# Optimization experiments

Hardware: AMD Instinct MI355X
Metric: run time of the kernel (lower is better)

Reference implementation:

```python
import jax, jax.numpy as jnp
import numpy as np

N = 100000   # nodes
E = 300000   # edges per snapshot
S = 5        # snapshots
D_IN = 128   # node_dim
H = 256      # hidden dim
P = 10000    # post nodes


def setup_inputs() -> dict:
    key = jax.random.key(0)
    ks = jax.random.split(key, 8)
    node_features = jax.random.normal(ks[0], (N, D_IN), jnp.float32)
    edge_index = jax.random.randint(ks[1], (S, 2, E), 0, N, dtype=jnp.int64)
    post_idx = jax.random.randint(ks[2], (P,), 0, N, dtype=jnp.int64)
    glorot = lambda k, sh, fan: jax.random.normal(k, sh, jnp.float32) * (1.0 / np.sqrt(fan))
    return {
        'node_features': node_features,
        'edge_index': edge_index,
        'post_idx': post_idx,
        'W1': glorot(ks[3], (D_IN, H), D_IN), 'b1': jnp.zeros((H,), jnp.float32),
        'W2': glorot(ks[4], (H, H), H),       'b2': jnp.zeros((H,), jnp.float32),
        'Wc1': glorot(ks[5], (H, H // 2), H), 'bc1': jnp.zeros((H // 2,), jnp.float32),
        'Wc2': glorot(ks[6], (H // 2, 1), H // 2), 'bc2': jnp.zeros((1,), jnp.float32),
    }


def gcn_conv(x, src, dst, W, b):
    """PyG GCNConv: h = D^-1/2 (A+I) D^-1/2 (x W) + b, aggregate at target (dst)."""
    n = x.shape[0]
    h = x @ W                                   # [n, out]
    loop = jnp.arange(n, dtype=src.dtype)
    src2 = jnp.concatenate([src, loop])          # add self-loops
    dst2 = jnp.concatenate([dst, loop])
    deg = jax.ops.segment_sum(jnp.ones_like(dst2, jnp.float32), dst2, num_segments=n)
    dinv = jnp.where(deg > 0, jax.lax.rsqrt(deg), 0.0)
    norm = dinv[src2] * dinv[dst2]               # [E+n]
    out = jax.ops.segment_sum(h[src2] * norm[:, None], dst2, num_segments=n)
    return out + b


def reference(node_features, edge_index, post_idx, W1, b1, W2, b2, Wc1, bc1, Wc2, bc2):
    embs = []
    for s in range(edge_index.shape[0]):  # loop over fixed small snapshot count
        src, dst = edge_index[s, 0], edge_index[s, 1]
        # layer 0: 128 -> 256, relu, no skip (dims differ)
        x1 = jax.nn.relu(gcn_conv(node_features, src, dst, W1, b1))
        # layer 1 (last): 256 -> 256, no relu, residual skip
        x2 = gcn_conv(x1, src, dst, W2, b2) + x1
        embs.append(x2)
    agg = jnp.mean(jnp.stack(embs, axis=0), axis=0)  # mean over snapshots
    post = agg[post_idx]                             # [P, H]
    logits = jax.nn.relu(post @ Wc1 + bc1) @ Wc2 + bc2
    return jax.nn.sigmoid(logits[:, 0])              # [P]
```

## Files before the change

### kernel.cpp

```cpp
#include <hip/hip_runtime.h>
#include <hip/hip_bf16.h>
#include <math.h>

#define NN 100000
#define NE 300000
#define NS 5
#define DIN 128
#define HID 256
#define NP 10000
#define NB_N 391

#define NBUCK 1024
#define NBUCK_USED 782
#define PBLK 64
#define EPB 19
#define BCAP 2048
#define CAPR 40960
#define NCPAD 16
#define LDB 136

typedef short s8v __attribute__((ext_vector_type(8)));
typedef float f4v __attribute__((ext_vector_type(4)));

static __device__ __forceinline__ float bf2f(unsigned short u) {
    union { unsigned int i; float f; } v; v.i = ((unsigned int)u) << 16; return v.f;
}
static __device__ __forceinline__ unsigned short f2bf(float f) {
    union { float f; unsigned int i; } v; v.f = f;
    return (unsigned short)((v.i + 0x7fff + ((v.i >> 16) & 1)) >> 16);
}


__global__ void setpost_kernel(const int* __restrict__ post, int* __restrict__ isPost,
                               int* __restrict__ needed) {
    int i = blockIdx.x * 256 + threadIdx.x;
    int s = blockIdx.y;
    if (i < NP) {
        int nd = post[i];
        needed[(size_t)s * NN + nd] = 1;
        if (s == 0) isPost[nd] = 1;
    }
}


__global__ void prep_kernel(const float* __restrict__ X, unsigned short* __restrict__ Xb,
                            const float* __restrict__ W1, unsigned short* __restrict__ W1t,
                            const float* __restrict__ W2, unsigned short* __restrict__ W2t,
                            const float* __restrict__ Wc1, unsigned short* __restrict__ Wc1t) {
    int b = blockIdx.x, t = threadIdx.x;
    if (b < 12500) {
        int i = b * 256 + t;
        float4 v = *(const float4*)&X[(size_t)i * 4];
        ushort4 o;
        o.x = f2bf(v.x); o.y = f2bf(v.y); o.z = f2bf(v.z); o.w = f2bf(v.w);
        *(ushort4*)&Xb[(size_t)i * 4] = o;
    } else if (b < 12628) {
        int i = (b - 12500) * 256 + t;
        int n = i >> 7, k = i & 127;
        W1t[i] = f2bf(W1[(size_t)k * 256 + n]);
    } else if (b < 12884) {
        int i = (b - 12628) * 256 + t;
        int n = i >> 8, k = i & 255;
        W2t[i] = f2bf(W2[(size_t)k * 256 + n]);
    } else {
        int i = (b - 12884) * 256 + t;
        int n = i >> 8, k = i & 255;
        Wc1t[i] = f2bf(Wc1[(size_t)k * 128 + n]);
    }
}


__global__ void hist_kernel(const int* __restrict__ EI, int* __restrict__ bhist) {
    __shared__ int h[NBUCK];
    int s = blockIdx.y, b = blockIdx.x, t = threadIdx.x;
    for (int q = t; q < NBUCK; q += 256) h[q] = 0;
    __syncthreads();
    const int* dstp = EI + (size_t)s * 2 * NE + NE;
    int e0 = b * (EPB * 256);
    #pragma unroll
    for (int j = 0; j < EPB; j++) {
        int e = e0 + j * 256 + t;
        if (e < NE) atomicAdd(&h[dstp[e] >> 7], 1);
    }
    __syncthreads();
    for (int q = t; q < NBUCK; q += 256)
        if (h[q]) atomicAdd(&bhist[s * NBUCK + q], h[q]);
}

__global__ void bscan_kernel(const int* __restrict__ bhist, int* __restrict__ bbase,
                             int* __restrict__ bcur) {
    __shared__ int sm[NBUCK];
    int s = blockIdx.x, t = threadIdx.x;
    int v = bhist[s * NBUCK + t];
    sm[t] = v;
    __syncthreads();
    for (int d = 1; d < NBUCK; d <<= 1) {
        int x = (t >= d) ? sm[t - d] : 0;
        __syncthreads();
        sm[t] += x;
        __syncthreads();
    }
    int base = sm[t] - v;
    bbase[s * NBUCK + t] = base;
    bcur[s * NBUCK + t] = base;
}

__global__ void part_kernel(const int* __restrict__ EI, int* __restrict__ bcur,
                            int2* __restrict__ pairs) {
    __shared__ int h[NBUCK];
    __shared__ int base[NBUCK];
    int s = blockIdx.y, b = blockIdx.x, t = threadIdx.x;
    for (int q = t; q < NBUCK; q += 256) h[q] = 0;
    __syncthreads();
    const int* srcp = EI + (size_t)s * 2 * NE;
    const int* dstp = srcp + NE;
    int e0 = b * (EPB * 256);
    int rs[EPB], rd[EPB];
    #pragma unroll
    for (int j = 0; j < EPB; j++) {
        int e = e0 + j * 256 + t;
        if (e < NE) {
            rs[j] = srcp[e];
            rd[j] = dstp[e];
            atomicAdd(&h[rd[j] >> 7], 1);
        } else {
            rd[j] = -1; rs[j] = 0;
        }
    }
    __syncthreads();
    for (int q = t; q < NBUCK; q += 256) {
        int c = h[q];
        base[q] = c ? atomicAdd(&bcur[s * NBUCK + q], c) : 0;
    }
    __syncthreads();
    #pragma unroll
    for (int j = 0; j < EPB; j++) {
        if (rd[j] >= 0) {
            int pos = atomicAdd(&base[rd[j] >> 7], 1);
            pairs[(size_t)s * NE + pos] = make_int2(rs[j], rd[j]);
        }
    }
}

__global__ void bucket_csr_kernel(const int2* __restrict__ pairs, const int* __restrict__ bbase,
                                  const int* __restrict__ bhist, const int* __restrict__ isPost,
                                  int* __restrict__ cnt, int* __restrict__ offs,
                                  float* __restrict__ dinv, int* __restrict__ csr,
                                  int* __restrict__ needed) {
    __shared__ int nh[128];
    __shared__ int noff[128];
    __shared__ int sbuf[BCAP];
    int s = blockIdx.y, b = blockIdx.x, t = threadIdx.x;
    int base = bbase[s * NBUCK + b];
    int count = bhist[s * NBUCK + b];
    if (count > BCAP) count = BCAP;
    if (t < 128) nh[t] = 0;
    __syncthreads();
    const int2* pp = pairs + (size_t)s * NE + base;
    for (int e = t; e < count; e += 256)
        atomicAdd(&nh[pp[e].y & 127], 1);
    __syncthreads();
    if (t < 128) noff[t] = nh[t];
    __syncthreads();
    for (int d = 1; d < 128; d <<= 1) {
        int x = 0;
        if (t < 128 && t >= d) x = noff[t - d];
        __syncthreads();
        if (t < 128) noff[t] += x;
        __syncthreads();
    }
    if (t < 128) {
        int excl = noff[t] - nh[t];
        noff[t] = excl;
        int g = b * 128 + t;
        if (g < NN) {
            int c = nh[t];
            cnt[(size_t)s * NN + g]  = c;
            offs[(size_t)s * NN + g] = base + excl;
            dinv[(size_t)s * NN + g] = rsqrtf((float)(c + 1));
        }
    }
    __syncthreads();
    for (int e = t; e < count; e += 256) {
        int2 pr = pp[e];
        int pos = atomicAdd(&noff[pr.y & 127], 1);
        sbuf[pos] = pr.x;
        if (isPost[pr.y]) needed[(size_t)s * NN + pr.x] = 1;
    }
    __syncthreads();
    for (int e = t; e < count; e += 256)
        csr[(size_t)s * NE + base + e] = sbuf[e];
}


__global__ void compact_kernel(const int* __restrict__ needed, int* __restrict__ ncount,
                               int* __restrict__ list, int* __restrict__ inv) {
    __shared__ int wcnt[4];
    __shared__ int gbase;
    int s = blockIdx.y;
    int i = blockIdx.x * 256 + threadIdx.x;
    int wave = threadIdx.x >> 6, lane = threadIdx.x & 63;
    bool pred = (i < NN) && (needed[(size_t)s * NN + i] != 0);
    unsigned long long mask = __ballot(pred);
    int wc = __popcll(mask);
    if (lane == 0) wcnt[wave] = wc;
    __syncthreads();
    if (threadIdx.x == 0) {
        int tot = wcnt[0] + wcnt[1] + wcnt[2] + wcnt[3];
        gbase = tot ? atomicAdd(&ncount[s * NCPAD], tot) : 0;
    }
    __syncthreads();
    if (pred) {
        int wbase = gbase;
        #pragma unroll
        for (int q = 0; q < 4; q++) if (q < wave) wbase += wcnt[q];
        int rank = __popcll(mask & ((1ull << lane) - 1ull));
        int slot = wbase + rank;
        if (slot < CAPR) {
            list[(size_t)s * NN + slot] = i;
            inv[(size_t)s * NN + i] = slot;
        }
    }
}


__global__ __launch_bounds__(1024) void agg_mm1_kernel(
        const unsigned short* __restrict__ Xb, const unsigned short* __restrict__ W1t,
        const int* __restrict__ ncount, const float* __restrict__ dinvA,
        const int* __restrict__ offsA, const int* __restrict__ cntA,
        const int* __restrict__ csrA, const int* __restrict__ listA,
        const float* __restrict__ b1, unsigned short* __restrict__ x1cA) {
    int s = blockIdx.y;
    int M = ncount[s * NCPAD];
    if (M > CAPR) M = CAPR;
    if (blockIdx.x * 256 >= M) return;
    const float* dinv = dinvA + (size_t)s * NN;
    const int* offs = offsA + (size_t)s * NN;
    const int* cnt  = cntA + (size_t)s * NN;
    const int* csr  = csrA + (size_t)s * NE;
    const int* list = listA + (size_t)s * NN;
    unsigned short* x1c = x1cA + (size_t)s * CAPR * HID;

    __shared__ unsigned short ldsB[256 * LDB];
    int tid = threadIdx.x;
    for (int q = tid; q < 256 * 16; q += 1024) {
        int n = q >> 4;
        int k8 = (q & 15) * 8;
        *(s8v*)&ldsB[n * LDB + k8] = *(const s8v*)&W1t[n * 128 + k8];
    }
    __syncthreads();

    int wave = tid >> 6, lane = tid & 63, lr = lane & 15, g = lane >> 4;
    int rowbase = blockIdx.x * 256 + wave * 16;
    int arow = rowbase + lr;

    float ga[4][8];
    #pragma unroll
    for (int kk = 0; kk < 4; kk++)
        #pragma unroll
        for (int j = 0; j < 8; j++) ga[kk][j] = 0.f;
    float di = 0.f;

    if (arow < M) {
        int node = list[arow];
        int o = offs[node], c = cnt[node];
        di = dinv[node];
        const unsigned short* rp = Xb + (size_t)node * DIN + g * 8;
        #pragma unroll
        for (int kk = 0; kk < 4; kk++) {
            s8v h = *(const s8v*)(rp + kk * 32);
            #pragma unroll
            for (int j = 0; j < 8; j++) ga[kk][j] = di * bf2f((unsigned short)h[j]);
        }
        for (int k = 0; k < c; k++) {
            int sv = csr[o + k];
            float wgt = dinv[sv];
            const unsigned short* sp = Xb + (size_t)sv * DIN + g * 8;
            #pragma unroll
            for (int kk = 0; kk < 4; kk++) {
                s8v h = *(const s8v*)(sp + kk * 32);
                #pragma unroll
                for (int j = 0; j < 8; j++) ga[kk][j] += wgt * bf2f((unsigned short)h[j]);
            }
        }
    }

    f4v acc[16];
    #pragma unroll
    for (int t8 = 0; t8 < 16; t8++) acc[t8] = (f4v){0.f, 0.f, 0.f, 0.f};
    #pragma unroll
    for (int kk = 0; kk < 4; kk++) {
        s8v a;
        #pragma unroll
        for (int j = 0; j < 8; j++) a[j] = (short)f2bf(ga[kk][j]);
        #pragma unroll
        for (int t8 = 0; t8 < 16; t8++) {
            s8v b = *(const s8v*)&ldsB[(t8 * 16 + lr) * LDB + kk * 32 + g * 8];
            acc[t8] = __builtin_amdgcn_mfma_f32_16x16x32_bf16(a, b, acc[t8], 0, 0, 0);
        }
    }

    int orow0 = rowbase + g * 4;
    #pragma unroll
    for (int r = 0; r < 4; r++) {
        int row = orow0 + r;
        float sc = __shfl(di, g * 4 + r, 64);
        if (row < M) {
            #pragma unroll
            for (int t8 = 0; t8 < 16; t8++) {
                int col = t8 * 16 + lr;
                float v = sc * acc[t8][r] + b1[col];
                x1c[(size_t)row * HID + col] = f2bf(v > 0.f ? v : 0.f);
            }
        }
    }
}


__global__ void z2_kernel(const unsigned short* __restrict__ x1cA, const float* __restrict__ dinvA,
                          const int* __restrict__ offsA, const int* __restrict__ cntA,
                          const int* __restrict__ csrA, const int* __restrict__ invA,
                          const int* __restrict__ post, unsigned short* __restrict__ z2bA) {
    int s = blockIdx.y;
    const unsigned short* x1c = x1cA + (size_t)s * CAPR * HID;
    const float* dinv = dinvA + (size_t)s * NN;
    const int* offs = offsA + (size_t)s * NN;
    const int* cnt  = cntA + (size_t)s * NN;
    const int* csr  = csrA + (size_t)s * NE;
    const int* inv  = invA + (size_t)s * NN;
    unsigned short* z2b = z2bA + (size_t)s * NP * HID;

    int wave = threadIdx.x >> 6, lane = threadIdx.x & 63;
    int eg = lane >> 4, el = lane & 15;
    int p = blockIdx.x * 4 + wave;
    if (p >= NP) return;
    int node = post[p];
    int o = offs[node], c = cnt[node];
    float acc0[8] = {0.f, 0.f, 0.f, 0.f, 0.f, 0.f, 0.f, 0.f};
    float acc1[8] = {0.f, 0.f, 0.f, 0.f, 0.f, 0.f, 0.f, 0.f};
    for (int k = eg; k < c; k += 4) {
        int sv = csr[o + k];
        float wgt = dinv[sv];
        int r = inv[sv];
        const unsigned short* rp = &x1c[(size_t)r * HID + el * 16];
        s8v h0 = *(const s8v*)rp;
        s8v h1 = *(const s8v*)(rp + 8);
        #pragma unroll
        for (int j = 0; j < 8; j++) {
            acc0[j] += wgt * bf2f((unsigned short)h0[j]);
            acc1[j] += wgt * bf2f((unsigned short)h1[j]);
        }
    }
    if (eg == 0) {
        float di = dinv[node];
        int r = inv[node];
        const unsigned short* rp = &x1c[(size_t)r * HID + el * 16];
        s8v h0 = *(const s8v*)rp;
        s8v h1 = *(const s8v*)(rp + 8);
        #pragma unroll
        for (int j = 0; j < 8; j++) {
            acc0[j] += di * bf2f((unsigned short)h0[j]);
            acc1[j] += di * bf2f((unsigned short)h1[j]);
        }
    }
    #pragma unroll
    for (int j = 0; j < 8; j++) {
        acc0[j] += __shfl_xor(acc0[j], 16, 64);
        acc0[j] += __shfl_xor(acc0[j], 32, 64);
        acc1[j] += __shfl_xor(acc1[j], 16, 64);
        acc1[j] += __shfl_xor(acc1[j], 32, 64);
    }
    if (eg == 0) {
        s8v o0, o1;
        #pragma unroll
        for (int j = 0; j < 8; j++) {
            o0[j] = (short)f2bf(acc0[j]);
            o1[j] = (short)f2bf(acc1[j]);
        }
        unsigned short* wp = &z2b[(size_t)p * HID + el * 16];
        *(s8v*)wp = o0;
        *(s8v*)(wp + 8) = o1;
    }
}


__global__ __launch_bounds__(1024) void mm2_kernel(
        const unsigned short* __restrict__ z2bA,
        const unsigned short* __restrict__ W2t,
        const float* __restrict__ dinvA,
        const int* __restrict__ post,
        const int* __restrict__ invA,
        const float* __restrict__ b2,
        const unsigned short* __restrict__ x1cA,
        float* __restrict__ aggPA) {
    int s = blockIdx.z;
    const unsigned short* A = z2bA + (size_t)s * NP * HID;
    const float* dinv = dinvA + (size_t)s * NN;
    const int* inv = invA + (size_t)s * NN;
    const unsigned short* x1c = x1cA + (size_t)s * CAPR * HID;
    float* Out = aggPA + (size_t)s * NP * HID;

    __shared__ unsigned short lds[128 * (HID + 8)];
    int tid = threadIdx.x;
    int colbase = blockIdx.y * 128;
    for (int q = tid; q < 128 * 32; q += 1024) {
        int n = q >> 5;
        int k8 = (q & 31) * 8;
        *(s8v*)&lds[n * (HID + 8) + k8] = *(const s8v*)&W2t[(size_t)(colbase + n) * HID + k8];
    }
    __syncthreads();

    int wave = tid >> 6, lane = tid & 63, lr = lane & 15, g = lane >> 4;
    int rowbase = blockIdx.x * 256 + wave * 16;
    int arow = rowbase + lr;

    f4v acc[8];
    #pragma unroll
    for (int t = 0; t < 8; t++) acc[t] = (f4v){0.f, 0.f, 0.f, 0.f};

    #pragma unroll
    for (int kk = 0; kk < HID / 32; kk++) {
        s8v a = (s8v){0, 0, 0, 0, 0, 0, 0, 0};
        if (arow < NP) a = *(const s8v*)&A[(size_t)arow * HID + kk * 32 + g * 8];
        #pragma unroll
        for (int t = 0; t < 8; t++) {
            s8v b = *(const s8v*)&lds[(t * 16 + lr) * (HID + 8) + kk * 32 + g * 8];
            acc[t] = __builtin_amdgcn_mfma_f32_16x16x32_bf16(a, b, acc[t], 0, 0, 0);
        }
    }

    int orow0 = rowbase + g * 4;
    #pragma unroll
    for (int r = 0; r < 4; r++) {
        int row = orow0 + r;
        if (row < NP) {
            int nd = post[row];
            float sc = dinv[nd];
            size_t x1row = (size_t)inv[nd] * HID;
            #pragma unroll
            for (int t = 0; t < 8; t++) {
                int col = colbase + t * 16 + lr;
                Out[(size_t)row * HID + col] =
                    sc * acc[t][r] + b2[col] + bf2f(x1c[x1row + col]);
            }
        }
    }
}


__global__ void redcvt_kernel(const float* __restrict__ aggPA, unsigned short* __restrict__ aggPb) {
    int i = blockIdx.x * 256 + threadIdx.x;
    if (i < NP * HID / 4) {
        float4 a = *(const float4*)&aggPA[(size_t)i * 4];
        #pragma unroll
        for (int s = 1; s < NS; s++) {
            float4 b = *(const float4*)&aggPA[(size_t)s * NP * HID + (size_t)i * 4];
            a.x += b.x; a.y += b.y; a.z += b.z; a.w += b.w;
        }
        ushort4 o;
        o.x = f2bf(a.x); o.y = f2bf(a.y); o.z = f2bf(a.z); o.w = f2bf(a.w);
        *(ushort4*)&aggPb[(size_t)i * 4] = o;
    }
}


__global__ __launch_bounds__(256) void mm3f_kernel(
        const unsigned short* __restrict__ A, const unsigned short* __restrict__ Bt,
        const float* __restrict__ bc1, const float* __restrict__ Wc2,
        const float* __restrict__ bc2, float* __restrict__ out) {
    __shared__ float tile[64 * 133];
    __shared__ float wc2s[128];
    int tid = threadIdx.x;
    if (tid < 128) wc2s[tid] = Wc2[tid];
    int wave = tid >> 6, lane = tid & 63, lr = lane & 15, g = lane >> 4;
    int rowbase = blockIdx.x * 64 + wave * 16;
    int arow = rowbase + lr;

    f4v acc[8];
    #pragma unroll
    for (int t = 0; t < 8; t++) acc[t] = (f4v){0.f, 0.f, 0.f, 0.f};

    #pragma unroll
    for (int kk = 0; kk < HID / 32; kk++) {
        s8v a = (s8v){0, 0, 0, 0, 0, 0, 0, 0};
        if (arow < NP) a = *(const s8v*)&A[(size_t)arow * HID + kk * 32 + g * 8];
        #pragma unroll
        for (int t = 0; t < 8; t++) {
            s8v b = *(const s8v*)&Bt[(size_t)(t * 16 + lr) * HID + kk * 32 + g * 8];
            acc[t] = __builtin_amdgcn_mfma_f32_16x16x32_bf16(a, b, acc[t], 0, 0, 0);
        }
    }

    #pragma unroll
    for (int r = 0; r < 4; r++) {
        int lrow = wave * 16 + g * 4 + r;
        #pragma unroll
        for (int t = 0; t < 8; t++) {
            int col = t * 16 + lr;
            float v = 0.2f * acc[t][r] + bc1[col];
            tile[lrow * 133 + col] = v > 0.f ? v : 0.f;
        }
    }
    __syncthreads();

    int lrow = wave * 16 + (lane >> 2);
    int chunk = lane & 3;
    float ssum = 0.f;
    #pragma unroll
    for (int j = 0; j < 32; j++)
        ssum += tile[lrow * 133 + chunk + 4 * j] * wc2s[chunk + 4 * j];
    ssum += __shfl_xor(ssum, 1, 64);
    ssum += __shfl_xor(ssum, 2, 64);
    int p = blockIdx.x * 64 + lrow;
    if (chunk == 0 && p < NP)
        out[p] = 1.f / (1.f + expf(-(ssum + bc2[0])));
}


extern "C" void kernel_launch(void* const* d_in, const int* in_sizes, int n_in,
                              void* d_out, int out_size, void* d_ws, size_t ws_size,
                              hipStream_t stream) {
    const float* X    = (const float*)d_in[0];
    const int*   EI   = (const int*)d_in[1];
    const int*   post = (const int*)d_in[2];
    const float* W1   = (const float*)d_in[3];
    const float* b1   = (const float*)d_in[4];
    const float* W2   = (const float*)d_in[5];
    const float* b2   = (const float*)d_in[6];
    const float* Wc1  = (const float*)d_in[7];
    const float* bc1  = (const float*)d_in[8];
    const float* Wc2  = (const float*)d_in[9];
    const float* bc2  = (const float*)d_in[10];
    float* out = (float*)d_out;

    char* w = (char*)d_ws;
    auto carve = [&](size_t bytes) {
        void* p = (void*)w;
        w += (bytes + 255) & ~(size_t)255;
        return p;
    };
    unsigned short* Xb    = (unsigned short*)carve((size_t)NN * DIN * 2);
    unsigned short* x1c   = (unsigned short*)carve((size_t)NS * CAPR * HID * 2);
    unsigned short* z2b5  = (unsigned short*)carve((size_t)NS * NP * HID * 2);
    float* aggP5          = (float*)carve((size_t)NS * NP * HID * 4);
    unsigned short* aggPb = (unsigned short*)carve((size_t)NP * HID * 2);
    unsigned short* W1t   = (unsigned short*)carve((size_t)256 * 128 * 2);
    unsigned short* W2t   = (unsigned short*)carve((size_t)256 * 256 * 2);
    unsigned short* Wc1t  = (unsigned short*)carve((size_t)128 * 256 * 2);
    float* dinv           = (float*)carve((size_t)NS * NN * 4);
    int*   cnt            = (int*)carve((size_t)NS * NN * 4);
    int*   offs           = (int*)carve((size_t)NS * NN * 4);
    int*   needed         = (int*)carve((size_t)NS * NN * 4);
    int*   list           = (int*)carve((size_t)NS * NN * 4);
    int*   inv            = (int*)carve((size_t)NS * NN * 4);
    int*   isPost         = (int*)carve((size_t)NN * 4);
    int*   bhist          = (int*)carve((size_t)NS * NBUCK * 4);
    int*   bbase          = (int*)carve((size_t)NS * NBUCK * 4);
    int*   bcur           = (int*)carve((size_t)NS * NBUCK * 4);
    int*   ncount         = (int*)carve((size_t)NS * NCPAD * 4);
    int*   csr            = (int*)carve((size_t)NS * NE * 4);
    int2*  pairs          = (int2*)x1c;

    hipMemsetAsync(needed, 0, (size_t)NS * NN * 4, stream);
    hipMemsetAsync(isPost, 0, (size_t)NN * 4, stream);
    hipMemsetAsync(bhist, 0, (size_t)NS * NBUCK * 4, stream);
    hipMemsetAsync(ncount, 0, (size_t)NS * NCPAD * 4, stream);

    prep_kernel<<<13012, 256, 0, stream>>>(X, Xb, W1, W1t, W2, W2t, Wc1, Wc1t);
    setpost_kernel<<<dim3((NP + 255) / 256, NS), 256, 0, stream>>>(post, isPost, needed);

    hist_kernel<<<dim3(PBLK, NS), 256, 0, stream>>>(EI, bhist);
    bscan_kernel<<<NS, NBUCK, 0, stream>>>(bhist, bbase, bcur);
    part_kernel<<<dim3(PBLK, NS), 256, 0, stream>>>(EI, bcur, pairs);
    bucket_csr_kernel<<<dim3(NBUCK_USED, NS), 256, 0, stream>>>(pairs, bbase, bhist, isPost,
                                                                cnt, offs, dinv, csr, needed);
    compact_kernel<<<dim3(NB_N, NS), 256, 0, stream>>>(needed, ncount, list, inv);

    agg_mm1_kernel<<<dim3((CAPR + 255) / 256, NS), 1024, 0, stream>>>(
        Xb, W1t, ncount, dinv, offs, cnt, csr, list, b1, x1c);
    z2_kernel<<<dim3((NP + 3) / 4, NS), 256, 0, stream>>>(
        x1c, dinv, offs, cnt, csr, inv, post, z2b5);
    mm2_kernel<<<dim3((NP + 255) / 256, 2, NS), 1024, 0, stream>>>(
        z2b5, W2t, dinv, post, inv, b2, x1c, aggP5);

    redcvt_kernel<<<(NP * HID / 4 + 255) / 256, 256, 0, stream>>>(aggP5, aggPb);
    mm3f_kernel<<<(NP + 63) / 64, 256, 0, stream>>>(aggPb, Wc1t, bc1, Wc2, bc2, out);
}
```

Measured before the change: 232.1 us.

## Use fixed-capacity bucket slabs and fuse snapshot reduction into classifier GEMM

Drops the histogram and scan kernels for edge partitioning by giving each destination bucket a fixed slab of BCAP slots, so the counts come straight from the atomic cursors. It also removes the separate reduce-and-convert kernel and folds the five-snapshot sum and bf16 conversion into the A-operand loads of the classifier GEMM. Both changes cut kernel launches and one intermediate buffer round trip. The cost is a larger csr/pairs footprint. Any bucket holding more than BCAP edges is now silently truncated, and the pairs slab (SLAB per snapshot) must still fit inside the reused x1c region.

```diff
diff --git a/kernel.cpp b/kernel.cpp
--- a/kernel.cpp
+++ b/kernel.cpp
@@ -15,6 +15,7 @@
 #define PBLK 64
 #define EPB 19
 #define BCAP 2048
+#define SLAB (NBUCK * BCAP)
 #define CAPR 40960
 #define NCPAD 16
 #define LDB 136
@@ -70,39 +71,9 @@
 }
 
 
-__global__ void hist_kernel(const int* __restrict__ EI, int* __restrict__ bhist) {
-    __shared__ int h[NBUCK];
-    int s = blockIdx.y, b = blockIdx.x, t = threadIdx.x;
-    for (int q = t; q < NBUCK; q += 256) h[q] = 0;
-    __syncthreads();
-    const int* dstp = EI + (size_t)s * 2 * NE + NE;
-    int e0 = b * (EPB * 256);
-    #pragma unroll
-    for (int j = 0; j < EPB; j++) {
-        int e = e0 + j * 256 + t;
-        if (e < NE) atomicAdd(&h[dstp[e] >> 7], 1);
-    }
-    __syncthreads();
-    for (int q = t; q < NBUCK; q += 256)
-        if (h[q]) atomicAdd(&bhist[s * NBUCK + q], h[q]);
-}
-
-__global__ void bscan_kernel(const int* __restrict__ bhist, int* __restrict__ bbase,
-                             int* __restrict__ bcur) {
-    __shared__ int sm[NBUCK];
-    int s = blockIdx.x, t = threadIdx.x;
-    int v = bhist[s * NBUCK + t];
-    sm[t] = v;
-    __syncthreads();
-    for (int d = 1; d < NBUCK; d <<= 1) {
-        int x = (t >= d) ? sm[t - d] : 0;
-        __syncthreads();
-        sm[t] += x;
-        __syncthreads();
-    }
-    int base = sm[t] - v;
-    bbase[s * NBUCK + t] = base;
-    bcur[s * NBUCK + t] = base;
+__global__ void binit_kernel(int* __restrict__ bcur) {
+    int i = blockIdx.x * 256 + threadIdx.x;
+    if (i < NS * NBUCK) bcur[i] = (i % NBUCK) * BCAP;
 }
 
 __global__ void part_kernel(const int* __restrict__ EI, int* __restrict__ bcur,
@@ -137,13 +108,13 @@
     for (int j = 0; j < EPB; j++) {
         if (rd[j] >= 0) {
             int pos = atomicAdd(&base[rd[j] >> 7], 1);
-            pairs[(size_t)s * NE + pos] = make_int2(rs[j], rd[j]);
-        }
-    }
-}
-
-__global__ void bucket_csr_kernel(const int2* __restrict__ pairs, const int* __restrict__ bbase,
-                                  const int* __restrict__ bhist, const int* __restrict__ isPost,
+            pairs[(size_t)s * SLAB + pos] = make_int2(rs[j], rd[j]);
+        }
+    }
+}
+
+__global__ void bucket_csr_kernel(const int2* __restrict__ pairs, const int* __restrict__ bcur,
+                                  const int* __restrict__ isPost,
                                   int* __restrict__ cnt, int* __restrict__ offs,
                                   float* __restrict__ dinv, int* __restrict__ csr,
                                   int* __restrict__ needed) {
@@ -151,12 +122,12 @@
     __shared__ int noff[128];
     __shared__ int sbuf[BCAP];
     int s = blockIdx.y, b = blockIdx.x, t = threadIdx.x;
-    int base = bbase[s * NBUCK + b];
-    int count = bhist[s * NBUCK + b];
+    int base = b * BCAP;
+    int count = bcur[s * NBUCK + b] - base;
     if (count > BCAP) count = BCAP;
     if (t < 128) nh[t] = 0;
     __syncthreads();
-    const int2* pp = pairs + (size_t)s * NE + base;
+    const int2* pp = pairs + (size_t)s * SLAB + base;
     for (int e = t; e < count; e += 256)
         atomicAdd(&nh[pp[e].y & 127], 1);
     __syncthreads();
@@ -189,7 +160,7 @@
     }
     __syncthreads();
     for (int e = t; e < count; e += 256)
-        csr[(size_t)s * NE + base + e] = sbuf[e];
+        csr[(size_t)s * SLAB + base + e] = sbuf[e];
 }
 
 
@@ -237,7 +208,7 @@
     const float* dinv = dinvA + (size_t)s * NN;
     const int* offs = offsA + (size_t)s * NN;
     const int* cnt  = cntA + (size_t)s * NN;
-    const int* csr  = csrA + (size_t)s * NE;
+    const int* csr  = csrA + (size_t)s * SLAB;
     const int* list = listA + (size_t)s * NN;
     unsigned short* x1c = x1cA + (size_t)s * CAPR * HID;
 
@@ -326,7 +297,7 @@
     const float* dinv = dinvA + (size_t)s * NN;
     const int* offs = offsA + (size_t)s * NN;
     const int* cnt  = cntA + (size_t)s * NN;
-    const int* csr  = csrA + (size_t)s * NE;
+    const int* csr  = csrA + (size_t)s * SLAB;
     const int* inv  = invA + (size_t)s * NN;
     unsigned short* z2b = z2bA + (size_t)s * NP * HID;
 
@@ -448,24 +419,8 @@
 }
 
 
-__global__ void redcvt_kernel(const float* __restrict__ aggPA, unsigned short* __restrict__ aggPb) {
-    int i = blockIdx.x * 256 + threadIdx.x;
-    if (i < NP * HID / 4) {
-        float4 a = *(const float4*)&aggPA[(size_t)i * 4];
-        #pragma unroll
-        for (int s = 1; s < NS; s++) {
-            float4 b = *(const float4*)&aggPA[(size_t)s * NP * HID + (size_t)i * 4];
-            a.x += b.x; a.y += b.y; a.z += b.z; a.w += b.w;
-        }
-        ushort4 o;
-        o.x = f2bf(a.x); o.y = f2bf(a.y); o.z = f2bf(a.z); o.w = f2bf(a.w);
-        *(ushort4*)&aggPb[(size_t)i * 4] = o;
-    }
-}
-
-
 __global__ __launch_bounds__(256) void mm3f_kernel(
-        const unsigned short* __restrict__ A, const unsigned short* __restrict__ Bt,
+        const float* __restrict__ aggPA, const unsigned short* __restrict__ Bt,
         const float* __restrict__ bc1, const float* __restrict__ Wc2,
         const float* __restrict__ bc2, float* __restrict__ out) {
     __shared__ float tile[64 * 133];
@@ -483,7 +438,19 @@
     #pragma unroll
     for (int kk = 0; kk < HID / 32; kk++) {
         s8v a = (s8v){0, 0, 0, 0, 0, 0, 0, 0};
-        if (arow < NP) a = *(const s8v*)&A[(size_t)arow * HID + kk * 32 + g * 8];
+        if (arow < NP) {
+            float af[8] = {0.f, 0.f, 0.f, 0.f, 0.f, 0.f, 0.f, 0.f};
+            #pragma unroll
+            for (int s = 0; s < NS; s++) {
+                const float* Ap = aggPA + (size_t)s * NP * HID + (size_t)arow * HID + kk * 32 + g * 8;
+                float4 v0 = *(const float4*)Ap;
+                float4 v1 = *(const float4*)(Ap + 4);
+                af[0] += v0.x; af[1] += v0.y; af[2] += v0.z; af[3] += v0.w;
+                af[4] += v1.x; af[5] += v1.y; af[6] += v1.z; af[7] += v1.w;
+            }
+            #pragma unroll
+            for (int j = 0; j < 8; j++) a[j] = (short)f2bf(af[j]);
+        }
         #pragma unroll
         for (int t = 0; t < 8; t++) {
             s8v b = *(const s8v*)&Bt[(size_t)(t * 16 + lr) * HID + kk * 32 + g * 8];
@@ -543,7 +510,6 @@
     unsigned short* x1c   = (unsigned short*)carve((size_t)NS * CAPR * HID * 2);
     unsigned short* z2b5  = (unsigned short*)carve((size_t)NS * NP * HID * 2);
     float* aggP5          = (float*)carve((size_t)NS * NP * HID * 4);
-    unsigned short* aggPb = (unsigned short*)carve((size_t)NP * HID * 2);
     unsigned short* W1t   = (unsigned short*)carve((size_t)256 * 128 * 2);
     unsigned short* W2t   = (unsigned short*)carve((size_t)256 * 256 * 2);
     unsigned short* Wc1t  = (unsigned short*)carve((size_t)128 * 256 * 2);
@@ -554,25 +520,21 @@
     int*   list           = (int*)carve((size_t)NS * NN * 4);
     int*   inv            = (int*)carve((size_t)NS * NN * 4);
     int*   isPost         = (int*)carve((size_t)NN * 4);
-    int*   bhist          = (int*)carve((size_t)NS * NBUCK * 4);
-    int*   bbase          = (int*)carve((size_t)NS * NBUCK * 4);
     int*   bcur           = (int*)carve((size_t)NS * NBUCK * 4);
     int*   ncount         = (int*)carve((size_t)NS * NCPAD * 4);
-    int*   csr            = (int*)carve((size_t)NS * NE * 4);
+    int*   csr            = (int*)carve((size_t)NS * SLAB * 4);
     int2*  pairs          = (int2*)x1c;
 
     hipMemsetAsync(needed, 0, (size_t)NS * NN * 4, stream);
     hipMemsetAsync(isPost, 0, (size_t)NN * 4, stream);
-    hipMemsetAsync(bhist, 0, (size_t)NS * NBUCK * 4, stream);
     hipMemsetAsync(ncount, 0, (size_t)NS * NCPAD * 4, stream);
 
     prep_kernel<<<13012, 256, 0, stream>>>(X, Xb, W1, W1t, W2, W2t, Wc1, Wc1t);
     setpost_kernel<<<dim3((NP + 255) / 256, NS), 256, 0, stream>>>(post, isPost, needed);
 
-    hist_kernel<<<dim3(PBLK, NS), 256, 0, stream>>>(EI, bhist);
-    bscan_kernel<<<NS, NBUCK, 0, stream>>>(bhist, bbase, bcur);
+    binit_kernel<<<(NS * NBUCK + 255) / 256, 256, 0, stream>>>(bcur);
     part_kernel<<<dim3(PBLK, NS), 256, 0, stream>>>(EI, bcur, pairs);
-    bucket_csr_kernel<<<dim3(NBUCK_USED, NS), 256, 0, stream>>>(pairs, bbase, bhist, isPost,
+    bucket_csr_kernel<<<dim3(NBUCK_USED, NS), 256, 0, stream>>>(pairs, bcur, isPost,
                                                                 cnt, offs, dinv, csr, needed);
     compact_kernel<<<dim3(NB_N, NS), 256, 0, stream>>>(needed, ncount, list, inv);
 
@@ -583,6 +545,5 @@
     mm2_kernel<<<dim3((NP + 255) / 256, 2, NS), 1024, 0, stream>>>(
         z2b5, W2t, dinv, post, inv, b2, x1c, aggP5);
 
-    redcvt_kernel<<<(NP * HID / 4 + 255) / 256, 256, 0, stream>>>(aggP5, aggPb);
-    mm3f_kernel<<<(NP + 63) / 64, 256, 0, stream>>>(aggPb, Wc1t, bc1, Wc2, bc2, out);
-}
+    mm3f_kernel<<<(NP + 63) / 64, 256, 0, stream>>>(aggP5, Wc1t, bc1, Wc2, bc2, out);
+}
```

Result: faster. 221.5 us (-4.6%).
